# Kernel tuning notes

Hardware: AMD Instinct MI355X
Metric: run time of the kernel (lower is better)

Reference implementation:

```python
import jax, jax.numpy as jnp
import numpy as np

WS = (8, 8)
NUM_HEADS = 6
DIM = 192
HEAD_DIM = DIM // NUM_HEADS
SCALE = HEAD_DIM ** -0.5


def _relative_position_index(ws):
    ch, cw = np.arange(ws[0]), np.arange(ws[1])
    coords = np.stack(np.meshgrid(ch, cw, indexing='ij'))          # (2, Wh, Ww)
    cf = coords.reshape(2, -1)                                      # (2, N)
    rel = cf[:, :, None] - cf[:, None, :]                           # (2, N, N)
    rel = rel.transpose(1, 2, 0).copy()                             # (N, N, 2)
    rel[:, :, 0] += ws[0] - 1
    rel[:, :, 1] += ws[1] - 1
    rel[:, :, 0] *= 2 * ws[1] - 1
    return rel.sum(-1)                                              # (N, N)

REL_IDX = jnp.asarray(_relative_position_index(WS))


def setup_inputs() -> dict:
    key = jax.random.key(0)
    ks = jax.random.split(key, 9)
    B_, N, C = 8192, WS[0] * WS[1], DIM
    x1 = jax.random.normal(ks[0], (B_, N, C), jnp.float32)
    x2 = jax.random.normal(ks[1], (B_, N, C), jnp.float32)
    mask = jnp.zeros((1024, N, N), jnp.float32)
    q_w = jax.random.normal(ks[2], (C, C), jnp.float32) * 0.02
    q_b = jnp.zeros((C,), jnp.float32)
    kv_w = jax.random.normal(ks[3], (2 * C, C), jnp.float32) * 0.02
    kv_b = jnp.zeros((2 * C,), jnp.float32)
    proj_w = jax.random.normal(ks[4], (C, C), jnp.float32) * 0.02
    proj_b = jnp.zeros((C,), jnp.float32)
    table = jax.random.normal(ks[5], ((2 * WS[0] - 1) * (2 * WS[1] - 1), NUM_HEADS), jnp.float32) * 0.02
    return dict(x1=x1, x2=x2, mask=mask, q_w=q_w, q_b=q_b, kv_w=kv_w,
                kv_b=kv_b, proj_w=proj_w, proj_b=proj_b, table=table)


def reference(x1, x2, mask, q_w, q_b, kv_w, kv_b, proj_w, proj_b, table):
    B_, N, C = x1.shape
    H, hd = NUM_HEADS, HEAD_DIM
    q = (x1 @ q_w.T + q_b).reshape(B_, N, H, hd).transpose(0, 2, 1, 3)   # (B_,H,N,hd)
    kv = (x2 @ kv_w.T + kv_b).reshape(B_, N, 2, H, hd).transpose(2, 0, 3, 1, 4)
    k, v = kv[0], kv[1]                                                   # (B_,H,N,hd)
    attn = jnp.einsum('bhnd,bhmd->bhnm', q * SCALE, k)                    # (B_,H,N,N)
    bias = table[REL_IDX.reshape(-1)].reshape(N, N, H).transpose(2, 0, 1)  # (H,N,N)
    attn = attn + bias[None]
    nW = mask.shape[0]
    attn = attn.reshape(B_ // nW, nW, H, N, N) + mask[None, :, None]
    attn = jax.nn.softmax(attn.reshape(B_, H, N, N), axis=-1)
    out = jnp.einsum('bhnm,bhmd->bhnd', attn, v).transpose(0, 2, 1, 3).reshape(B_, N, C)
    return out @ proj_w.T + proj_b
```

## Files before the change

kernel.cpp:

```cpp
#include <hip/hip_runtime.h>

typedef __bf16 bf16_t;
typedef __bf16 bf16x8 __attribute__((ext_vector_type(8)));
typedef __bf16 bf16x4 __attribute__((ext_vector_type(4)));
typedef __bf16 bf16x2 __attribute__((ext_vector_type(2)));
typedef float f32x4 __attribute__((ext_vector_type(4)));

#define SCALE 0.17677669529663687f

__device__ __forceinline__ f32x4 mfma16(bf16x8 a, bf16x8 b, f32x4 c) {
  return __builtin_amdgcn_mfma_f32_16x16x32_bf16(a, b, c, 0, 0, 0);
}

__device__ __forceinline__ int swz(int row, int colByte, int strideB) {
  return row * strideB + ((((colByte >> 4) ^ (row & 7)) << 4) | (colByte & 15));
}

__device__ __forceinline__ void barrier_nd() {
  asm volatile("s_waitcnt lgkmcnt(0)" ::: "memory");
  __builtin_amdgcn_s_barrier();
  asm volatile("" ::: "memory");
}

union CvtU { bf16x2 h; unsigned int u; };
union PaU { unsigned int u[4]; bf16x8 v; };

__global__ void prep(const float* __restrict__ qw, const float* __restrict__ kvw,
                     const float* __restrict__ pw, bf16_t* __restrict__ wsb) {
  int i = blockIdx.x * 256 + threadIdx.x;
#pragma unroll
  for (int j = 0; j < 4; ++j) {
    int e = i * 4 + j;
    float v;
    if (e < 36864) v = qw[e] * SCALE;
    else if (e < 110592) v = kvw[e - 36864];
    else v = pw[e - 110592];
    wsb[e] = (bf16_t)v;
  }
}

template <bool WS>
__device__ __forceinline__ bf16x8 ldw(const bf16_t* __restrict__ wb,
                                      const float* __restrict__ wf, int off) {
  if constexpr (WS) {
    return *(const bf16x8*)(wb + off);
  } else {
    const float4* p = (const float4*)(wf + off);
    float4 a = p[0], c = p[1];
    bf16x8 r;
    r[0] = (bf16_t)a.x; r[1] = (bf16_t)a.y; r[2] = (bf16_t)a.z; r[3] = (bf16_t)a.w;
    r[4] = (bf16_t)c.x; r[5] = (bf16_t)c.y; r[6] = (bf16_t)c.z; r[7] = (bf16_t)c.w;
    return r;
  }
}

template <bool WS>
__global__ __launch_bounds__(512, 2) void wca_main(
    const float* __restrict__ x1, const float* __restrict__ x2,
    const float* __restrict__ mask,
    const float* __restrict__ qw_f, const float* __restrict__ qb,
    const float* __restrict__ kvw_f, const float* __restrict__ kvb,
    const float* __restrict__ pw_f, const float* __restrict__ pb,
    const float* __restrict__ table,
    const bf16_t* __restrict__ wsb,
    float* __restrict__ out) {
  extern __shared__ char smem[];
  char* RA = smem;
  char* RK = smem + 49152;
  char* RV = smem + 98304;

  const int t = threadIdx.x;
  const int w = t >> 6, l = t & 63, lo = l & 15, hi = l >> 4;
  const int win0 = 2 * blockIdx.x;

  const bf16_t* q_wb = wsb;
  const bf16_t* kv_wb = wsb + 36864;
  const bf16_t* p_wb = wsb + 110592;

  {
    const float4* s2a = (const float4*)(x2 + (size_t)win0 * 12288);
    const float4* s2b = (const float4*)(x2 + (size_t)(win0 + 1) * 12288);
    float4 ld[12];
#pragma unroll
    for (int it = 0; it < 3; ++it) {
      int idx = it * 512 + t;
      ld[4 * it + 0] = s2a[2 * idx]; ld[4 * it + 1] = s2a[2 * idx + 1];
      ld[4 * it + 2] = s2b[2 * idx]; ld[4 * it + 3] = s2b[2 * idx + 1];
    }
#pragma unroll
    for (int it = 0; it < 3; ++it) {
      int idx = it * 512 + t;
      int n = idx / 24, g = idx - n * 24;
      bf16x8 v;
      float4 a = ld[4 * it + 0], c = ld[4 * it + 1];
      v[0] = (bf16_t)a.x; v[1] = (bf16_t)a.y; v[2] = (bf16_t)a.z; v[3] = (bf16_t)a.w;
      v[4] = (bf16_t)c.x; v[5] = (bf16_t)c.y; v[6] = (bf16_t)c.z; v[7] = (bf16_t)c.w;
      *(bf16x8*)(RA + swz(n, g * 16, 384)) = v;
      a = ld[4 * it + 2]; c = ld[4 * it + 3];
      v[0] = (bf16_t)a.x; v[1] = (bf16_t)a.y; v[2] = (bf16_t)a.z; v[3] = (bf16_t)a.w;
      v[4] = (bf16_t)c.x; v[5] = (bf16_t)c.y; v[6] = (bf16_t)c.z; v[7] = (bf16_t)c.w;
      *(bf16x8*)(RA + swz(64 + n, g * 16, 384)) = v;
    }
  }
  barrier_nd();

  {
    bf16x8 wA[6][3];
#pragma unroll
    for (int kk = 0; kk < 6; ++kk)
#pragma unroll
      for (int ct = 0; ct < 3; ++ct) {
        int row = w * 48 + ct * 16 + lo;
        wA[kk][ct] = ldw<WS>(kv_wb, kvw_f, row * 192 + kk * 32 + hi * 8);
      }
    for (int wv = 0; wv < 2; ++wv) {
      f32x4 acc[4][3];
#pragma unroll
      for (int rt = 0; rt < 4; ++rt)
#pragma unroll
        for (int ct = 0; ct < 3; ++ct) { f32x4 z = {0.f, 0.f, 0.f, 0.f}; acc[rt][ct] = z; }
#pragma unroll
      for (int kk = 0; kk < 6; ++kk) {
        bf16x8 a[4];
#pragma unroll
        for (int rt = 0; rt < 4; ++rt)
          a[rt] = *(const bf16x8*)(RA + swz(wv * 64 + rt * 16 + lo, (kk * 4 + hi) * 16, 384));
#pragma unroll
        for (int rt = 0; rt < 4; ++rt)
#pragma unroll
          for (int ct = 0; ct < 3; ++ct)
            acc[rt][ct] = mfma16(a[rt], wA[kk][ct], acc[rt][ct]);
      }
      if (w < 4) {
#pragma unroll
        for (int ct = 0; ct < 3; ++ct) {
          int och = w * 48 + ct * 16 + lo;
          float bv = kvb[och];
#pragma unroll
          for (int rt = 0; rt < 4; ++rt)
#pragma unroll
            for (int i = 0; i < 4; ++i)
              *(bf16_t*)(RK + swz(wv * 64 + rt * 16 + hi * 4 + i, och * 2, 384)) =
                  (bf16_t)(acc[rt][ct][i] + bv);
        }
      } else {
#pragma unroll
        for (int ct = 0; ct < 3; ++ct) {
          int och = (w - 4) * 48 + ct * 16 + lo;
          float bv = kvb[192 + och];
#pragma unroll
          for (int rt = 0; rt < 4; ++rt) {
            int n0 = rt * 16 + hi * 4;
            bf16x4 pk;
#pragma unroll
            for (int i = 0; i < 4; ++i) pk[i] = (bf16_t)(acc[rt][ct][i] + bv);
            *(bf16x4*)(RV + wv * 24576 + swz(och, n0 * 2, 128)) = pk;
          }
        }
      }
    }
  }
  barrier_nd();

  {
    const int wv = w >> 2, rt2 = (w >> 1) & 1, cg = w & 1;
    const float* x1w = x1 + (size_t)(win0 + wv) * 12288;
    f32x4 acc[2][6];
#pragma unroll
    for (int rt = 0; rt < 2; ++rt)
#pragma unroll
      for (int ct = 0; ct < 6; ++ct) { f32x4 z = {0.f, 0.f, 0.f, 0.f}; acc[rt][ct] = z; }
#pragma unroll
    for (int kh = 0; kh < 2; ++kh) {
      float4 xf[2][3][2];
#pragma unroll
      for (int rt = 0; rt < 2; ++rt) {
        const float4* p = (const float4*)(x1w + (rt2 * 32 + rt * 16 + lo) * 192);
#pragma unroll
        for (int k2 = 0; k2 < 3; ++k2) {
          xf[rt][k2][0] = p[(kh * 3 + k2) * 8 + hi * 2];
          xf[rt][k2][1] = p[(kh * 3 + k2) * 8 + hi * 2 + 1];
        }
      }
      bf16x8 wB[3][6];
#pragma unroll
      for (int k2 = 0; k2 < 3; ++k2)
#pragma unroll
        for (int ct = 0; ct < 6; ++ct) {
          int col = cg * 96 + ct * 16 + lo;
          wB[k2][ct] = ldw<WS>(q_wb, qw_f, col * 192 + (kh * 3 + k2) * 32 + hi * 8);
        }
#pragma unroll
      for (int k2 = 0; k2 < 3; ++k2)
#pragma unroll
        for (int rt = 0; rt < 2; ++rt) {
          bf16x8 a;
          float4 xa = xf[rt][k2][0], xb = xf[rt][k2][1];
          a[0] = (bf16_t)xa.x; a[1] = (bf16_t)xa.y; a[2] = (bf16_t)xa.z; a[3] = (bf16_t)xa.w;
          a[4] = (bf16_t)xb.x; a[5] = (bf16_t)xb.y; a[6] = (bf16_t)xb.z; a[7] = (bf16_t)xb.w;
#pragma unroll
          for (int ct = 0; ct < 6; ++ct) acc[rt][ct] = mfma16(a, wB[k2][ct], acc[rt][ct]);
        }
    }
#pragma unroll
    for (int ct = 0; ct < 6; ++ct) {
      int col = cg * 96 + ct * 16 + lo;
      float qbs = qb[col] * SCALE;
#pragma unroll
      for (int rt = 0; rt < 2; ++rt)
#pragma unroll
        for (int i = 0; i < 4; ++i) {
          int row = wv * 64 + rt2 * 32 + rt * 16 + hi * 4 + i;
          float val = WS ? (acc[rt][ct][i] + qbs) : (acc[rt][ct][i] + qb[col]) * SCALE;
          *(bf16_t*)(RA + swz(row, col * 2, 384)) = (bf16_t)val;
        }
    }
  }
  barrier_nd();

  {
    const int wv = w >> 2, rt32 = (w >> 1) & 1, hh = w & 1;
    const int win = win0 + wv;
    const float* maskb = mask + (size_t)(win & 1023) * 4096;
    f32x4 mk[2][4];
    int ridx[2][4][4];
#pragma unroll
    for (int rts = 0; rts < 2; ++rts) {
      int r = rt32 * 32 + rts * 16 + lo;
#pragma unroll
      for (int ct = 0; ct < 4; ++ct) {
        mk[rts][ct] = *(const f32x4*)(maskb + r * 64 + ct * 16 + hi * 4);
#pragma unroll
        for (int i = 0; i < 4; ++i) {
          int c = ct * 16 + hi * 4 + i;
          ridx[rts][ct][i] = (((r >> 3) - (c >> 3) + 7) * 15 + ((r & 7) - (c & 7) + 7)) * 6;
        }
      }
    }
#pragma unroll
    for (int hq = 0; hq < 3; ++hq) {
      const int h = hh * 3 + hq;
#pragma unroll
      for (int rts = 0; rts < 2; ++rts) {
        const int rbase = rt32 * 32 + rts * 16;
        const int r = rbase + lo;
        bf16x8 qa = *(const bf16x8*)(RA + swz(wv * 64 + r, h * 64 + hi * 16, 384));
        f32x4 s[4];
#pragma unroll
        for (int ct = 0; ct < 4; ++ct) {
          f32x4 ci;
#pragma unroll
          for (int i = 0; i < 4; ++i) ci[i] = table[ridx[rts][ct][i] + h];
          ci += mk[rts][ct];
          bf16x8 ka = *(const bf16x8*)(RK + swz(wv * 64 + ct * 16 + lo, h * 64 + hi * 16, 384));
          s[ct] = mfma16(ka, qa, ci);
        }
        float mx = -1e30f;
#pragma unroll
        for (int ct = 0; ct < 4; ++ct)
#pragma unroll
          for (int i = 0; i < 4; ++i) mx = fmaxf(mx, s[ct][i]);
        mx = fmaxf(mx, __shfl_xor(mx, 16));
        mx = fmaxf(mx, __shfl_xor(mx, 32));
        float sum = 0.f;
#pragma unroll
        for (int ct = 0; ct < 4; ++ct)
#pragma unroll
          for (int i = 0; i < 4; ++i) {
            float p = __expf(s[ct][i] - mx);
            s[ct][i] = p;
            sum += p;
          }
        sum += __shfl_xor(sum, 16);
        sum += __shfl_xor(sum, 32);
        float rinv = 1.0f / sum;
        unsigned int word[4][2];
#pragma unroll
        for (int ct = 0; ct < 4; ++ct)
#pragma unroll
          for (int i2 = 0; i2 < 2; ++i2) {
            CvtU cu;
            cu.h[0] = (bf16_t)(s[ct][2 * i2] * rinv);
            cu.h[1] = (bf16_t)(s[ct][2 * i2 + 1] * rinv);
            word[ct][i2] = cu.u;
          }
        f32x4 o0 = {0.f, 0.f, 0.f, 0.f}, o1 = {0.f, 0.f, 0.f, 0.f};
#pragma unroll
        for (int k2 = 0; k2 < 2; ++k2) {
          PaU pa;
#pragma unroll
          for (int j2 = 0; j2 < 4; ++j2) {
            int src = lo + ((hi & 1) << 5) + ((j2 >> 1) << 4);
            unsigned int wa = (unsigned int)__shfl((int)word[2 * k2][j2 & 1], src);
            unsigned int wb = (unsigned int)__shfl((int)word[2 * k2 + 1][j2 & 1], src);
            pa.u[j2] = (hi & 2) ? wb : wa;
          }
          bf16x8 v0 = *(const bf16x8*)(RV + wv * 24576 + swz(h * 32 + lo, k2 * 64 + hi * 16, 128));
          bf16x8 v1 = *(const bf16x8*)(RV + wv * 24576 + swz(h * 32 + 16 + lo, k2 * 64 + hi * 16, 128));
          o0 = mfma16(pa.v, v0, o0);
          o1 = mfma16(pa.v, v1, o1);
        }
#pragma unroll
        for (int i = 0; i < 4; ++i) {
          int rr = wv * 64 + rbase + hi * 4 + i;
          *(bf16_t*)(RA + swz(rr, h * 64 + lo * 2, 384)) = (bf16_t)o0[i];
          *(bf16_t*)(RA + swz(rr, h * 64 + 32 + lo * 2, 384)) = (bf16_t)o1[i];
        }
      }
    }
  }
  barrier_nd();

  {
    const int wv = w >> 2, cgo = w & 3;
    bf16x8 wO[6][3];
#pragma unroll
    for (int kk = 0; kk < 6; ++kk)
#pragma unroll
      for (int ct = 0; ct < 3; ++ct) {
        int col = cgo * 48 + ct * 16 + lo;
        wO[kk][ct] = ldw<WS>(p_wb, pw_f, col * 192 + kk * 32 + hi * 8);
      }
    f32x4 acc[4][3];
#pragma unroll
    for (int rt = 0; rt < 4; ++rt)
#pragma unroll
      for (int ct = 0; ct < 3; ++ct) { f32x4 z = {0.f, 0.f, 0.f, 0.f}; acc[rt][ct] = z; }
#pragma unroll
    for (int kk = 0; kk < 6; ++kk) {
      bf16x8 a[4];
#pragma unroll
      for (int rt = 0; rt < 4; ++rt)
        a[rt] = *(const bf16x8*)(RA + swz(wv * 64 + rt * 16 + lo, (kk * 4 + hi) * 16, 384));
#pragma unroll
      for (int rt = 0; rt < 4; ++rt)
#pragma unroll
        for (int ct = 0; ct < 3; ++ct)
          acc[rt][ct] = mfma16(a[rt], wO[kk][ct], acc[rt][ct]);
    }
    float* outp = out + (size_t)(win0 + wv) * 12288;
#pragma unroll
    for (int ct = 0; ct < 3; ++ct) {
      int col = cgo * 48 + ct * 16 + lo;
      float bv = pb[col];
#pragma unroll
      for (int rt = 0; rt < 4; ++rt)
#pragma unroll
        for (int i = 0; i < 4; ++i)
          outp[(rt * 16 + hi * 4 + i) * 192 + col] = acc[rt][ct][i] + bv;
    }
  }
}

extern "C" void kernel_launch(void* const* d_in, const int* in_sizes, int n_in,
                              void* d_out, int out_size, void* d_ws, size_t ws_size,
                              hipStream_t stream) {
  const float* x1 = (const float*)d_in[0];
  const float* x2 = (const float*)d_in[1];
  const float* mask = (const float*)d_in[2];
  const float* qw = (const float*)d_in[3];
  const float* qb = (const float*)d_in[4];
  const float* kvw = (const float*)d_in[5];
  const float* kvb = (const float*)d_in[6];
  const float* pw = (const float*)d_in[7];
  const float* pb = (const float*)d_in[8];
  const float* table = (const float*)d_in[9];
  float* out = (float*)d_out;
  bf16_t* wsb = (bf16_t*)d_ws;
  const int LDS_BYTES = 147456;
  if (ws_size >= 294912) {
    prep<<<144, 256, 0, stream>>>(qw, kvw, pw, wsb);
    wca_main<true><<<4096, 512, LDS_BYTES, stream>>>(x1, x2, mask, qw, qb, kvw, kvb,
                                                     pw, pb, table, wsb, out);
  } else {
    wca_main<false><<<4096, 512, LDS_BYTES, stream>>>(x1, x2, mask, qw, qb, kvw, kvb,
                                                      pw, pb, table, wsb, out);
  }
}
```

Measured before the change: 651.9 us.

## Prefetch x1 during KV GEMM, transpose MFMA outputs for vector LDS stores, drop barrier

Half of the x1 tile for the Q projection is now loaded into registers during the KV projection phase, so its global latency overlaps with that phase's MFMAs. The mask loads are moved into the Q GEMM. Several MFMAs swap operand order so each lane holds four consecutive columns, which turns scalar bf16 LDS stores into packed bf16x4 stores for K, Q and attention output. The barrier between Q projection and attention is removed, since each wave now reads only the Q rows it wrote itself. This adds register pressure under launch_bounds(512,2), and the relative-position indices are recomputed inline instead of being precomputed.

```diff
diff --git a/kernel.cpp b/kernel.cpp
--- a/kernel.cpp
+++ b/kernel.cpp
@@ -72,6 +72,7 @@
   const int t = threadIdx.x;
   const int w = t >> 6, l = t & 63, lo = l & 15, hi = l >> 4;
   const int win0 = 2 * blockIdx.x;
+  const int wvB = w >> 2, rt2 = (w >> 1) & 1, hh = w & 1;
 
   const bf16_t* q_wb = wsb;
   const bf16_t* kv_wb = wsb + 36864;
@@ -104,15 +105,30 @@
   }
   barrier_nd();
 
+  float4 xp[12];
   {
+    const int part = w >> 2;
+    const int kcol = (w & 3) * 48;
     bf16x8 wA[6][3];
 #pragma unroll
     for (int kk = 0; kk < 6; ++kk)
 #pragma unroll
       for (int ct = 0; ct < 3; ++ct) {
-        int row = w * 48 + ct * 16 + lo;
+        int row = part * 192 + kcol + ct * 16 + lo;
         wA[kk][ct] = ldw<WS>(kv_wb, kvw_f, row * 192 + kk * 32 + hi * 8);
       }
+    {
+      const float* x1w = x1 + (size_t)(win0 + wvB) * 12288;
+#pragma unroll
+      for (int rt = 0; rt < 2; ++rt) {
+        const float4* p = (const float4*)(x1w + (rt2 * 32 + rt * 16 + lo) * 192);
+#pragma unroll
+        for (int k2 = 0; k2 < 3; ++k2) {
+          xp[rt * 6 + k2 * 2 + 0] = p[k2 * 8 + hi * 2];
+          xp[rt * 6 + k2 * 2 + 1] = p[k2 * 8 + hi * 2 + 1];
+        }
+      }
+    }
     for (int wv = 0; wv < 2; ++wv) {
       f32x4 acc[4][3];
 #pragma unroll
@@ -125,28 +141,37 @@
 #pragma unroll
         for (int rt = 0; rt < 4; ++rt)
           a[rt] = *(const bf16x8*)(RA + swz(wv * 64 + rt * 16 + lo, (kk * 4 + hi) * 16, 384));
-#pragma unroll
-        for (int rt = 0; rt < 4; ++rt)
-#pragma unroll
-          for (int ct = 0; ct < 3; ++ct)
-            acc[rt][ct] = mfma16(a[rt], wA[kk][ct], acc[rt][ct]);
-      }
-      if (w < 4) {
+        if (part == 0) {
+#pragma unroll
+          for (int rt = 0; rt < 4; ++rt)
+#pragma unroll
+            for (int ct = 0; ct < 3; ++ct)
+              acc[rt][ct] = mfma16(wA[kk][ct], a[rt], acc[rt][ct]);
+        } else {
+#pragma unroll
+          for (int rt = 0; rt < 4; ++rt)
+#pragma unroll
+            for (int ct = 0; ct < 3; ++ct)
+              acc[rt][ct] = mfma16(a[rt], wA[kk][ct], acc[rt][ct]);
+        }
+      }
+      if (part == 0) {
 #pragma unroll
         for (int ct = 0; ct < 3; ++ct) {
-          int och = w * 48 + ct * 16 + lo;
-          float bv = kvb[och];
-#pragma unroll
-          for (int rt = 0; rt < 4; ++rt)
-#pragma unroll
-            for (int i = 0; i < 4; ++i)
-              *(bf16_t*)(RK + swz(wv * 64 + rt * 16 + hi * 4 + i, och * 2, 384)) =
-                  (bf16_t)(acc[rt][ct][i] + bv);
+          f32x4 bv4 = *(const f32x4*)(kvb + kcol + ct * 16 + hi * 4);
+#pragma unroll
+          for (int rt = 0; rt < 4; ++rt) {
+            bf16x4 pk;
+#pragma unroll
+            for (int i = 0; i < 4; ++i) pk[i] = (bf16_t)(acc[rt][ct][i] + bv4[i]);
+            *(bf16x4*)(RK + swz(wv * 64 + rt * 16 + lo,
+                                kcol * 2 + ct * 32 + hi * 8, 384)) = pk;
+          }
         }
       } else {
 #pragma unroll
         for (int ct = 0; ct < 3; ++ct) {
-          int och = (w - 4) * 48 + ct * 16 + lo;
+          int och = kcol + ct * 16 + lo;
           float bv = kvb[192 + och];
 #pragma unroll
           for (int rt = 0; rt < 4; ++rt) {
@@ -162,97 +187,117 @@
   }
   barrier_nd();
 
+  f32x4 mk[2][4];
   {
-    const int wv = w >> 2, rt2 = (w >> 1) & 1, cg = w & 1;
-    const float* x1w = x1 + (size_t)(win0 + wv) * 12288;
+    const float* x1w = x1 + (size_t)(win0 + wvB) * 12288;
+    float4 xq[12];
+#pragma unroll
+    for (int rt = 0; rt < 2; ++rt) {
+      const float4* p = (const float4*)(x1w + (rt2 * 32 + rt * 16 + lo) * 192);
+#pragma unroll
+      for (int k2 = 0; k2 < 3; ++k2) {
+        xq[rt * 6 + k2 * 2 + 0] = p[(3 + k2) * 8 + hi * 2];
+        xq[rt * 6 + k2 * 2 + 1] = p[(3 + k2) * 8 + hi * 2 + 1];
+      }
+    }
     f32x4 acc[2][6];
 #pragma unroll
     for (int rt = 0; rt < 2; ++rt)
 #pragma unroll
       for (int ct = 0; ct < 6; ++ct) { f32x4 z = {0.f, 0.f, 0.f, 0.f}; acc[rt][ct] = z; }
-#pragma unroll
-    for (int kh = 0; kh < 2; ++kh) {
-      float4 xf[2][3][2];
-#pragma unroll
-      for (int rt = 0; rt < 2; ++rt) {
-        const float4* p = (const float4*)(x1w + (rt2 * 32 + rt * 16 + lo) * 192);
-#pragma unroll
-        for (int k2 = 0; k2 < 3; ++k2) {
-          xf[rt][k2][0] = p[(kh * 3 + k2) * 8 + hi * 2];
-          xf[rt][k2][1] = p[(kh * 3 + k2) * 8 + hi * 2 + 1];
-        }
-      }
+    {
       bf16x8 wB[3][6];
 #pragma unroll
       for (int k2 = 0; k2 < 3; ++k2)
 #pragma unroll
         for (int ct = 0; ct < 6; ++ct) {
-          int col = cg * 96 + ct * 16 + lo;
-          wB[k2][ct] = ldw<WS>(q_wb, qw_f, col * 192 + (kh * 3 + k2) * 32 + hi * 8);
+          int col = hh * 96 + ct * 16 + lo;
+          wB[k2][ct] = ldw<WS>(q_wb, qw_f, col * 192 + k2 * 32 + hi * 8);
         }
 #pragma unroll
       for (int k2 = 0; k2 < 3; ++k2)
 #pragma unroll
         for (int rt = 0; rt < 2; ++rt) {
+          float4 xa = xp[rt * 6 + k2 * 2], xb = xp[rt * 6 + k2 * 2 + 1];
           bf16x8 a;
-          float4 xa = xf[rt][k2][0], xb = xf[rt][k2][1];
           a[0] = (bf16_t)xa.x; a[1] = (bf16_t)xa.y; a[2] = (bf16_t)xa.z; a[3] = (bf16_t)xa.w;
           a[4] = (bf16_t)xb.x; a[5] = (bf16_t)xb.y; a[6] = (bf16_t)xb.z; a[7] = (bf16_t)xb.w;
 #pragma unroll
-          for (int ct = 0; ct < 6; ++ct) acc[rt][ct] = mfma16(a, wB[k2][ct], acc[rt][ct]);
+          for (int ct = 0; ct < 6; ++ct)
+            acc[rt][ct] = mfma16(wB[k2][ct], a, acc[rt][ct]);
+        }
+    }
+    {
+      const float* maskb = mask + (size_t)((win0 + wvB) & 1023) * 4096;
+#pragma unroll
+      for (int rts = 0; rts < 2; ++rts) {
+        int r = rt2 * 32 + rts * 16 + lo;
+#pragma unroll
+        for (int ct = 0; ct < 4; ++ct)
+          mk[rts][ct] = *(const f32x4*)(maskb + r * 64 + ct * 16 + hi * 4);
+      }
+    }
+    {
+      bf16x8 wB[3][6];
+#pragma unroll
+      for (int k2 = 0; k2 < 3; ++k2)
+#pragma unroll
+        for (int ct = 0; ct < 6; ++ct) {
+          int col = hh * 96 + ct * 16 + lo;
+          wB[k2][ct] = ldw<WS>(q_wb, qw_f, col * 192 + (3 + k2) * 32 + hi * 8);
+        }
+#pragma unroll
+      for (int k2 = 0; k2 < 3; ++k2)
+#pragma unroll
+        for (int rt = 0; rt < 2; ++rt) {
+          float4 xa = xq[rt * 6 + k2 * 2], xb = xq[rt * 6 + k2 * 2 + 1];
+          bf16x8 a;
+          a[0] = (bf16_t)xa.x; a[1] = (bf16_t)xa.y; a[2] = (bf16_t)xa.z; a[3] = (bf16_t)xa.w;
+          a[4] = (bf16_t)xb.x; a[5] = (bf16_t)xb.y; a[6] = (bf16_t)xb.z; a[7] = (bf16_t)xb.w;
+#pragma unroll
+          for (int ct = 0; ct < 6; ++ct)
+            acc[rt][ct] = mfma16(wB[k2][ct], a, acc[rt][ct]);
         }
     }
 #pragma unroll
     for (int ct = 0; ct < 6; ++ct) {
-      int col = cg * 96 + ct * 16 + lo;
-      float qbs = qb[col] * SCALE;
-#pragma unroll
-      for (int rt = 0; rt < 2; ++rt)
+      f32x4 qb4 = *(const f32x4*)(qb + hh * 96 + ct * 16 + hi * 4);
+#pragma unroll
+      for (int rt = 0; rt < 2; ++rt) {
+        int row = wvB * 64 + rt2 * 32 + rt * 16 + lo;
+        bf16x4 pk;
 #pragma unroll
         for (int i = 0; i < 4; ++i) {
-          int row = wv * 64 + rt2 * 32 + rt * 16 + hi * 4 + i;
-          float val = WS ? (acc[rt][ct][i] + qbs) : (acc[rt][ct][i] + qb[col]) * SCALE;
-          *(bf16_t*)(RA + swz(row, col * 2, 384)) = (bf16_t)val;
-        }
-    }
-  }
-  barrier_nd();
+          float val = WS ? (acc[rt][ct][i] + qb4[i] * SCALE)
+                         : (acc[rt][ct][i] + qb4[i]) * SCALE;
+          pk[i] = (bf16_t)val;
+        }
+        *(bf16x4*)(RA + swz(row, hh * 192 + ct * 32 + hi * 8, 384)) = pk;
+      }
+    }
+  }
 
   {
-    const int wv = w >> 2, rt32 = (w >> 1) & 1, hh = w & 1;
-    const int win = win0 + wv;
-    const float* maskb = mask + (size_t)(win & 1023) * 4096;
-    f32x4 mk[2][4];
-    int ridx[2][4][4];
-#pragma unroll
-    for (int rts = 0; rts < 2; ++rts) {
-      int r = rt32 * 32 + rts * 16 + lo;
-#pragma unroll
-      for (int ct = 0; ct < 4; ++ct) {
-        mk[rts][ct] = *(const f32x4*)(maskb + r * 64 + ct * 16 + hi * 4);
-#pragma unroll
-        for (int i = 0; i < 4; ++i) {
-          int c = ct * 16 + hi * 4 + i;
-          ridx[rts][ct][i] = (((r >> 3) - (c >> 3) + 7) * 15 + ((r & 7) - (c & 7) + 7)) * 6;
-        }
-      }
-    }
 #pragma unroll
     for (int hq = 0; hq < 3; ++hq) {
       const int h = hh * 3 + hq;
 #pragma unroll
       for (int rts = 0; rts < 2; ++rts) {
-        const int rbase = rt32 * 32 + rts * 16;
+        const int rbase = rt2 * 32 + rts * 16;
         const int r = rbase + lo;
-        bf16x8 qa = *(const bf16x8*)(RA + swz(wv * 64 + r, h * 64 + hi * 16, 384));
+        bf16x8 qa = *(const bf16x8*)(RA + swz(wvB * 64 + r, h * 64 + hi * 16, 384));
         f32x4 s[4];
 #pragma unroll
         for (int ct = 0; ct < 4; ++ct) {
           f32x4 ci;
 #pragma unroll
-          for (int i = 0; i < 4; ++i) ci[i] = table[ridx[rts][ct][i] + h];
+          for (int i = 0; i < 4; ++i) {
+            int c = ct * 16 + hi * 4 + i;
+            int rel = (((r >> 3) - (c >> 3) + 7) * 15 + ((r & 7) - (c & 7) + 7)) * 6;
+            ci[i] = table[rel + h];
+          }
           ci += mk[rts][ct];
-          bf16x8 ka = *(const bf16x8*)(RK + swz(wv * 64 + ct * 16 + lo, h * 64 + hi * 16, 384));
+          bf16x8 ka = *(const bf16x8*)(RK + swz(wvB * 64 + ct * 16 + lo, h * 64 + hi * 16, 384));
           s[ct] = mfma16(ka, qa, ci);
         }
         float mx = -1e30f;
@@ -295,17 +340,16 @@
             unsigned int wb = (unsigned int)__shfl((int)word[2 * k2 + 1][j2 & 1], src);
             pa.u[j2] = (hi & 2) ? wb : wa;
           }
-          bf16x8 v0 = *(const bf16x8*)(RV + wv * 24576 + swz(h * 32 + lo, k2 * 64 + hi * 16, 128));
-          bf16x8 v1 = *(const bf16x8*)(RV + wv * 24576 + swz(h * 32 + 16 + lo, k2 * 64 + hi * 16, 128));
-          o0 = mfma16(pa.v, v0, o0);
-          o1 = mfma16(pa.v, v1, o1);
-        }
-#pragma unroll
-        for (int i = 0; i < 4; ++i) {
-          int rr = wv * 64 + rbase + hi * 4 + i;
-          *(bf16_t*)(RA + swz(rr, h * 64 + lo * 2, 384)) = (bf16_t)o0[i];
-          *(bf16_t*)(RA + swz(rr, h * 64 + 32 + lo * 2, 384)) = (bf16_t)o1[i];
-        }
+          bf16x8 v0 = *(const bf16x8*)(RV + wvB * 24576 + swz(h * 32 + lo, k2 * 64 + hi * 16, 128));
+          bf16x8 v1 = *(const bf16x8*)(RV + wvB * 24576 + swz(h * 32 + 16 + lo, k2 * 64 + hi * 16, 128));
+          o0 = mfma16(v0, pa.v, o0);
+          o1 = mfma16(v1, pa.v, o1);
+        }
+        bf16x4 p0, p1;
+#pragma unroll
+        for (int i = 0; i < 4; ++i) { p0[i] = (bf16_t)o0[i]; p1[i] = (bf16_t)o1[i]; }
+        *(bf16x4*)(RA + swz(wvB * 64 + r, h * 64 + hi * 8, 384)) = p0;
+        *(bf16x4*)(RA + swz(wvB * 64 + r, h * 64 + 32 + hi * 8, 384)) = p1;
       }
     }
   }
```

Result: slower. 720.7 us (+10.5%).

## Make kernel persistent with producer warps double-buffering next window's inputs

Applied to the files above, without the earlier changes.

Replaces the one-block-per-two-windows launch with 256 persistent blocks that each loop over 32 windows. Two warps act as producers, converting the next window's x1/x2 to bf16 in double-buffered LDS while six compute warps run KV projection, Q projection, attention and output projection on the current window. This aims to overlap global-load latency with MFMA work and to amortize launch and setup costs. In exchange it drops to 256 blocks, which may leave CUs underused on a 256-CU part at two blocks per CU. Compute warps also reload weights every iteration, and only six of eight warps do math.

```diff
diff --git a/kernel.cpp b/kernel.cpp
--- a/kernel.cpp
+++ b/kernel.cpp
@@ -65,88 +65,92 @@
     const bf16_t* __restrict__ wsb,
     float* __restrict__ out) {
   extern __shared__ char smem[];
-  char* RA = smem;
-  char* RK = smem + 49152;
-  char* RV = smem + 98304;
+  char* RK = smem + 98304;
+  char* RV = smem + 122880;
 
   const int t = threadIdx.x;
   const int w = t >> 6, l = t & 63, lo = l & 15, hi = l >> 4;
-  const int win0 = 2 * blockIdx.x;
+  const int bid = blockIdx.x;
 
   const bf16_t* q_wb = wsb;
   const bf16_t* kv_wb = wsb + 36864;
   const bf16_t* p_wb = wsb + 110592;
 
-  {
-    const float4* s2a = (const float4*)(x2 + (size_t)win0 * 12288);
-    const float4* s2b = (const float4*)(x2 + (size_t)(win0 + 1) * 12288);
-    float4 ld[12];
-#pragma unroll
-    for (int it = 0; it < 3; ++it) {
-      int idx = it * 512 + t;
-      ld[4 * it + 0] = s2a[2 * idx]; ld[4 * it + 1] = s2a[2 * idx + 1];
-      ld[4 * it + 2] = s2b[2 * idx]; ld[4 * it + 3] = s2b[2 * idx + 1];
+  const int rb = (w >= 3 && w < 6) ? 1 : 0;
+  const int cg3 = w - rb * 3;
+
+  if (w >= 6) {
+    const int L = (w - 6) * 64 + l;
+    const float4* s2 = (const float4*)(x2 + (size_t)(bid * 32) * 12288);
+    const float4* s1 = (const float4*)(x1 + (size_t)(bid * 32) * 12288);
+#pragma unroll
+    for (int ch = 0; ch < 12; ++ch) {
+      int G = ch * 128 + L;
+      int n = G / 24, g = G - n * 24;
+      float4 a = s2[2 * G], b = s2[2 * G + 1];
+      bf16x8 v;
+      v[0] = (bf16_t)a.x; v[1] = (bf16_t)a.y; v[2] = (bf16_t)a.z; v[3] = (bf16_t)a.w;
+      v[4] = (bf16_t)b.x; v[5] = (bf16_t)b.y; v[6] = (bf16_t)b.z; v[7] = (bf16_t)b.w;
+      *(bf16x8*)(smem + swz(n, g * 16, 384)) = v;
+      a = s1[2 * G]; b = s1[2 * G + 1];
+      v[0] = (bf16_t)a.x; v[1] = (bf16_t)a.y; v[2] = (bf16_t)a.z; v[3] = (bf16_t)a.w;
+      v[4] = (bf16_t)b.x; v[5] = (bf16_t)b.y; v[6] = (bf16_t)b.z; v[7] = (bf16_t)b.w;
+      *(bf16x8*)(smem + 49152 + swz(n, g * 16, 384)) = v;
     }
-#pragma unroll
-    for (int it = 0; it < 3; ++it) {
-      int idx = it * 512 + t;
-      int n = idx / 24, g = idx - n * 24;
-      bf16x8 v;
-      float4 a = ld[4 * it + 0], c = ld[4 * it + 1];
-      v[0] = (bf16_t)a.x; v[1] = (bf16_t)a.y; v[2] = (bf16_t)a.z; v[3] = (bf16_t)a.w;
-      v[4] = (bf16_t)c.x; v[5] = (bf16_t)c.y; v[6] = (bf16_t)c.z; v[7] = (bf16_t)c.w;
-      *(bf16x8*)(RA + swz(n, g * 16, 384)) = v;
-      a = ld[4 * it + 2]; c = ld[4 * it + 3];
-      v[0] = (bf16_t)a.x; v[1] = (bf16_t)a.y; v[2] = (bf16_t)a.z; v[3] = (bf16_t)a.w;
-      v[4] = (bf16_t)c.x; v[5] = (bf16_t)c.y; v[6] = (bf16_t)c.z; v[7] = (bf16_t)c.w;
-      *(bf16x8*)(RA + swz(64 + n, g * 16, 384)) = v;
-    }
   }
   barrier_nd();
 
-  {
-    bf16x8 wA[6][3];
-#pragma unroll
-    for (int kk = 0; kk < 6; ++kk)
-#pragma unroll
-      for (int ct = 0; ct < 3; ++ct) {
-        int row = w * 48 + ct * 16 + lo;
-        wA[kk][ct] = ldw<WS>(kv_wb, kvw_f, row * 192 + kk * 32 + hi * 8);
-      }
-    for (int wv = 0; wv < 2; ++wv) {
-      f32x4 acc[4][3];
+#pragma unroll 1
+  for (int j = 0; j < 32; ++j) {
+    const int win = bid * 32 + j;
+    const int cur = j & 1;
+    char* xin = smem + cur * 24576;
+    const char* x1s = smem + 49152 + cur * 24576;
+
+    if (w < 6) {
+      const int part = (w >= 3) ? 1 : 0;
+      const int kcol = cg3 * 64;
+      bf16x8 wA[6][4];
+#pragma unroll
+      for (int kk = 0; kk < 6; ++kk)
+#pragma unroll
+        for (int ct = 0; ct < 4; ++ct) {
+          int row = part * 192 + kcol + ct * 16 + lo;
+          wA[kk][ct] = ldw<WS>(kv_wb, kvw_f, row * 192 + kk * 32 + hi * 8);
+        }
+      f32x4 acc[4][4];
 #pragma unroll
       for (int rt = 0; rt < 4; ++rt)
 #pragma unroll
-        for (int ct = 0; ct < 3; ++ct) { f32x4 z = {0.f, 0.f, 0.f, 0.f}; acc[rt][ct] = z; }
+        for (int ct = 0; ct < 4; ++ct) { f32x4 z = {0.f, 0.f, 0.f, 0.f}; acc[rt][ct] = z; }
 #pragma unroll
       for (int kk = 0; kk < 6; ++kk) {
         bf16x8 a[4];
 #pragma unroll
         for (int rt = 0; rt < 4; ++rt)
-          a[rt] = *(const bf16x8*)(RA + swz(wv * 64 + rt * 16 + lo, (kk * 4 + hi) * 16, 384));
+          a[rt] = *(const bf16x8*)(xin + swz(rt * 16 + lo, (kk * 4 + hi) * 16, 384));
 #pragma unroll
         for (int rt = 0; rt < 4; ++rt)
 #pragma unroll
-          for (int ct = 0; ct < 3; ++ct)
+          for (int ct = 0; ct < 4; ++ct)
             acc[rt][ct] = mfma16(a[rt], wA[kk][ct], acc[rt][ct]);
       }
-      if (w < 4) {
-#pragma unroll
-        for (int ct = 0; ct < 3; ++ct) {
-          int och = w * 48 + ct * 16 + lo;
+      if (part == 0) {
+#pragma unroll
+        for (int ct = 0; ct < 4; ++ct) {
+          int och = kcol + ct * 16 + lo;
           float bv = kvb[och];
 #pragma unroll
           for (int rt = 0; rt < 4; ++rt)
 #pragma unroll
             for (int i = 0; i < 4; ++i)
-              *(bf16_t*)(RK + swz(wv * 64 + rt * 16 + hi * 4 + i, och * 2, 384)) =
+              *(bf16_t*)(RK + swz(rt * 16 + hi * 4 + i, och * 2, 384)) =
                   (bf16_t)(acc[rt][ct][i] + bv);
         }
       } else {
 #pragma unroll
-        for (int ct = 0; ct < 3; ++ct) {
-          int och = (w - 4) * 48 + ct * 16 + lo;
+        for (int ct = 0; ct < 4; ++ct) {
+          int och = kcol + ct * 16 + lo;
           float bv = kvb[192 + och];
 #pragma unroll
           for (int rt = 0; rt < 4; ++rt) {
@@ -154,200 +158,204 @@
             bf16x4 pk;
 #pragma unroll
             for (int i = 0; i < 4; ++i) pk[i] = (bf16_t)(acc[rt][ct][i] + bv);
-            *(bf16x4*)(RV + wv * 24576 + swz(och, n0 * 2, 128)) = pk;
+            *(bf16x4*)(RV + swz(och, n0 * 2, 128)) = pk;
           }
         }
       }
     }
-  }
-  barrier_nd();
-
-  {
-    const int wv = w >> 2, rt2 = (w >> 1) & 1, cg = w & 1;
-    const float* x1w = x1 + (size_t)(win0 + wv) * 12288;
-    f32x4 acc[2][6];
-#pragma unroll
-    for (int rt = 0; rt < 2; ++rt)
-#pragma unroll
-      for (int ct = 0; ct < 6; ++ct) { f32x4 z = {0.f, 0.f, 0.f, 0.f}; acc[rt][ct] = z; }
-#pragma unroll
-    for (int kh = 0; kh < 2; ++kh) {
-      float4 xf[2][3][2];
-#pragma unroll
-      for (int rt = 0; rt < 2; ++rt) {
-        const float4* p = (const float4*)(x1w + (rt2 * 32 + rt * 16 + lo) * 192);
-#pragma unroll
-        for (int k2 = 0; k2 < 3; ++k2) {
-          xf[rt][k2][0] = p[(kh * 3 + k2) * 8 + hi * 2];
-          xf[rt][k2][1] = p[(kh * 3 + k2) * 8 + hi * 2 + 1];
-        }
-      }
-      bf16x8 wB[3][6];
-#pragma unroll
-      for (int k2 = 0; k2 < 3; ++k2)
-#pragma unroll
-        for (int ct = 0; ct < 6; ++ct) {
-          int col = cg * 96 + ct * 16 + lo;
-          wB[k2][ct] = ldw<WS>(q_wb, qw_f, col * 192 + (kh * 3 + k2) * 32 + hi * 8);
-        }
-#pragma unroll
-      for (int k2 = 0; k2 < 3; ++k2)
-#pragma unroll
-        for (int rt = 0; rt < 2; ++rt) {
-          bf16x8 a;
-          float4 xa = xf[rt][k2][0], xb = xf[rt][k2][1];
-          a[0] = (bf16_t)xa.x; a[1] = (bf16_t)xa.y; a[2] = (bf16_t)xa.z; a[3] = (bf16_t)xa.w;
-          a[4] = (bf16_t)xb.x; a[5] = (bf16_t)xb.y; a[6] = (bf16_t)xb.z; a[7] = (bf16_t)xb.w;
-#pragma unroll
-          for (int ct = 0; ct < 6; ++ct) acc[rt][ct] = mfma16(a, wB[k2][ct], acc[rt][ct]);
-        }
+    barrier_nd();
+
+    if (w < 6) {
+      {
+        bf16x8 wB[6][4];
+#pragma unroll
+        for (int kk = 0; kk < 6; ++kk)
+#pragma unroll
+          for (int ct = 0; ct < 4; ++ct) {
+            int col = cg3 * 64 + ct * 16 + lo;
+            wB[kk][ct] = ldw<WS>(q_wb, qw_f, col * 192 + kk * 32 + hi * 8);
+          }
+        f32x4 acc[2][4];
+#pragma unroll
+        for (int rt = 0; rt < 2; ++rt)
+#pragma unroll
+          for (int ct = 0; ct < 4; ++ct) { f32x4 z = {0.f, 0.f, 0.f, 0.f}; acc[rt][ct] = z; }
+#pragma unroll
+        for (int kk = 0; kk < 6; ++kk) {
+          bf16x8 a[2];
+#pragma unroll
+          for (int rt = 0; rt < 2; ++rt)
+            a[rt] = *(const bf16x8*)(x1s + swz(rb * 32 + rt * 16 + lo, (kk * 4 + hi) * 16, 384));
+#pragma unroll
+          for (int rt = 0; rt < 2; ++rt)
+#pragma unroll
+            for (int ct = 0; ct < 4; ++ct)
+              acc[rt][ct] = mfma16(a[rt], wB[kk][ct], acc[rt][ct]);
+        }
+#pragma unroll
+        for (int ct = 0; ct < 4; ++ct) {
+          int col = cg3 * 64 + ct * 16 + lo;
+          float qv = qb[col];
+#pragma unroll
+          for (int rt = 0; rt < 2; ++rt)
+#pragma unroll
+            for (int i = 0; i < 4; ++i) {
+              int row = rb * 32 + rt * 16 + hi * 4 + i;
+              float val = WS ? (acc[rt][ct][i] + qv * SCALE)
+                             : (acc[rt][ct][i] + qv) * SCALE;
+              *(bf16_t*)(xin + swz(row, col * 2, 384)) = (bf16_t)val;
+            }
+        }
+      }
+      {
+        const float* maskb = mask + (size_t)(win & 1023) * 4096;
+        f32x4 mk[2][4];
+        int ridx[2][4][4];
+#pragma unroll
+        for (int rts = 0; rts < 2; ++rts) {
+          int r = rb * 32 + rts * 16 + lo;
+#pragma unroll
+          for (int ct = 0; ct < 4; ++ct) {
+            mk[rts][ct] = *(const f32x4*)(maskb + r * 64 + ct * 16 + hi * 4);
+#pragma unroll
+            for (int i = 0; i < 4; ++i) {
+              int cc = ct * 16 + hi * 4 + i;
+              ridx[rts][ct][i] = (((r >> 3) - (cc >> 3) + 7) * 15 + ((r & 7) - (cc & 7) + 7)) * 6;
+            }
+          }
+        }
+#pragma unroll
+        for (int hq = 0; hq < 2; ++hq) {
+          const int h = cg3 * 2 + hq;
+#pragma unroll
+          for (int rts = 0; rts < 2; ++rts) {
+            const int rbase = rb * 32 + rts * 16;
+            const int r = rbase + lo;
+            bf16x8 qa = *(const bf16x8*)(xin + swz(r, h * 64 + hi * 16, 384));
+            f32x4 s[4];
+#pragma unroll
+            for (int ct = 0; ct < 4; ++ct) {
+              f32x4 ci;
+#pragma unroll
+              for (int i = 0; i < 4; ++i) ci[i] = table[ridx[rts][ct][i] + h];
+              ci += mk[rts][ct];
+              bf16x8 ka = *(const bf16x8*)(RK + swz(ct * 16 + lo, h * 64 + hi * 16, 384));
+              s[ct] = mfma16(ka, qa, ci);
+            }
+            float mx = -1e30f;
+#pragma unroll
+            for (int ct = 0; ct < 4; ++ct)
+#pragma unroll
+              for (int i = 0; i < 4; ++i) mx = fmaxf(mx, s[ct][i]);
+            mx = fmaxf(mx, __shfl_xor(mx, 16));
+            mx = fmaxf(mx, __shfl_xor(mx, 32));
+            float sum = 0.f;
+#pragma unroll
+            for (int ct = 0; ct < 4; ++ct)
+#pragma unroll
+              for (int i = 0; i < 4; ++i) {
+                float p = __expf(s[ct][i] - mx);
+                s[ct][i] = p;
+                sum += p;
+              }
+            sum += __shfl_xor(sum, 16);
+            sum += __shfl_xor(sum, 32);
+            float rinv = 1.0f / sum;
+            unsigned int word[4][2];
+#pragma unroll
+            for (int ct = 0; ct < 4; ++ct)
+#pragma unroll
+              for (int i2 = 0; i2 < 2; ++i2) {
+                CvtU cu;
+                cu.h[0] = (bf16_t)(s[ct][2 * i2] * rinv);
+                cu.h[1] = (bf16_t)(s[ct][2 * i2 + 1] * rinv);
+                word[ct][i2] = cu.u;
+              }
+            f32x4 o0 = {0.f, 0.f, 0.f, 0.f}, o1 = {0.f, 0.f, 0.f, 0.f};
+#pragma unroll
+            for (int k2 = 0; k2 < 2; ++k2) {
+              PaU pa;
+#pragma unroll
+              for (int j2 = 0; j2 < 4; ++j2) {
+                int src = lo + ((hi & 1) << 5) + ((j2 >> 1) << 4);
+                unsigned int wa = (unsigned int)__shfl((int)word[2 * k2][j2 & 1], src);
+                unsigned int wb = (unsigned int)__shfl((int)word[2 * k2 + 1][j2 & 1], src);
+                pa.u[j2] = (hi & 2) ? wb : wa;
+              }
+              bf16x8 v0 = *(const bf16x8*)(RV + swz(h * 32 + lo, k2 * 64 + hi * 16, 128));
+              bf16x8 v1 = *(const bf16x8*)(RV + swz(h * 32 + 16 + lo, k2 * 64 + hi * 16, 128));
+              o0 = mfma16(pa.v, v0, o0);
+              o1 = mfma16(pa.v, v1, o1);
+            }
+#pragma unroll
+            for (int i = 0; i < 4; ++i) {
+              int rr = rbase + hi * 4 + i;
+              *(bf16_t*)(xin + swz(rr, h * 64 + lo * 2, 384)) = (bf16_t)o0[i];
+              *(bf16_t*)(xin + swz(rr, h * 64 + 32 + lo * 2, 384)) = (bf16_t)o1[i];
+            }
+          }
+        }
+      }
+    } else if (j < 31) {
+      const int L = (w - 6) * 64 + l;
+      char* xd = smem + (cur ^ 1) * 24576;
+      char* x1d = smem + 49152 + (cur ^ 1) * 24576;
+      const float4* s2 = (const float4*)(x2 + (size_t)(win + 1) * 12288);
+      const float4* s1 = (const float4*)(x1 + (size_t)(win + 1) * 12288);
+#pragma unroll
+      for (int ch = 0; ch < 12; ++ch) {
+        int G = ch * 128 + L;
+        int n = G / 24, g = G - n * 24;
+        float4 a = s2[2 * G], b = s2[2 * G + 1];
+        bf16x8 v;
+        v[0] = (bf16_t)a.x; v[1] = (bf16_t)a.y; v[2] = (bf16_t)a.z; v[3] = (bf16_t)a.w;
+        v[4] = (bf16_t)b.x; v[5] = (bf16_t)b.y; v[6] = (bf16_t)b.z; v[7] = (bf16_t)b.w;
+        *(bf16x8*)(xd + swz(n, g * 16, 384)) = v;
+        a = s1[2 * G]; b = s1[2 * G + 1];
+        v[0] = (bf16_t)a.x; v[1] = (bf16_t)a.y; v[2] = (bf16_t)a.z; v[3] = (bf16_t)a.w;
+        v[4] = (bf16_t)b.x; v[5] = (bf16_t)b.y; v[6] = (bf16_t)b.z; v[7] = (bf16_t)b.w;
+        *(bf16x8*)(x1d + swz(n, g * 16, 384)) = v;
+      }
     }
-#pragma unroll
-    for (int ct = 0; ct < 6; ++ct) {
-      int col = cg * 96 + ct * 16 + lo;
-      float qbs = qb[col] * SCALE;
+    barrier_nd();
+
+    if (w < 6) {
+      bf16x8 wO[6][4];
+#pragma unroll
+      for (int kk = 0; kk < 6; ++kk)
+#pragma unroll
+        for (int ct = 0; ct < 4; ++ct) {
+          int col = cg3 * 64 + ct * 16 + lo;
+          wO[kk][ct] = ldw<WS>(p_wb, pw_f, col * 192 + kk * 32 + hi * 8);
+        }
+      f32x4 acc[2][4];
 #pragma unroll
       for (int rt = 0; rt < 2; ++rt)
 #pragma unroll
-        for (int i = 0; i < 4; ++i) {
-          int row = wv * 64 + rt2 * 32 + rt * 16 + hi * 4 + i;
-          float val = WS ? (acc[rt][ct][i] + qbs) : (acc[rt][ct][i] + qb[col]) * SCALE;
-          *(bf16_t*)(RA + swz(row, col * 2, 384)) = (bf16_t)val;
-        }
-    }
-  }
-  barrier_nd();
-
-  {
-    const int wv = w >> 2, rt32 = (w >> 1) & 1, hh = w & 1;
-    const int win = win0 + wv;
-    const float* maskb = mask + (size_t)(win & 1023) * 4096;
-    f32x4 mk[2][4];
-    int ridx[2][4][4];
-#pragma unroll
-    for (int rts = 0; rts < 2; ++rts) {
-      int r = rt32 * 32 + rts * 16 + lo;
+        for (int ct = 0; ct < 4; ++ct) { f32x4 z = {0.f, 0.f, 0.f, 0.f}; acc[rt][ct] = z; }
+#pragma unroll
+      for (int kk = 0; kk < 6; ++kk) {
+        bf16x8 a[2];
+#pragma unroll
+        for (int rt = 0; rt < 2; ++rt)
+          a[rt] = *(const bf16x8*)(xin + swz(rb * 32 + rt * 16 + lo, (kk * 4 + hi) * 16, 384));
+#pragma unroll
+        for (int rt = 0; rt < 2; ++rt)
+#pragma unroll
+          for (int ct = 0; ct < 4; ++ct)
+            acc[rt][ct] = mfma16(a[rt], wO[kk][ct], acc[rt][ct]);
+      }
+      float* outp = out + (size_t)win * 12288;
 #pragma unroll
       for (int ct = 0; ct < 4; ++ct) {
-        mk[rts][ct] = *(const f32x4*)(maskb + r * 64 + ct * 16 + hi * 4);
-#pragma unroll
-        for (int i = 0; i < 4; ++i) {
-          int c = ct * 16 + hi * 4 + i;
-          ridx[rts][ct][i] = (((r >> 3) - (c >> 3) + 7) * 15 + ((r & 7) - (c & 7) + 7)) * 6;
-        }
-      }
-    }
-#pragma unroll
-    for (int hq = 0; hq < 3; ++hq) {
-      const int h = hh * 3 + hq;
-#pragma unroll
-      for (int rts = 0; rts < 2; ++rts) {
-        const int rbase = rt32 * 32 + rts * 16;
-        const int r = rbase + lo;
-        bf16x8 qa = *(const bf16x8*)(RA + swz(wv * 64 + r, h * 64 + hi * 16, 384));
-        f32x4 s[4];
-#pragma unroll
-        for (int ct = 0; ct < 4; ++ct) {
-          f32x4 ci;
-#pragma unroll
-          for (int i = 0; i < 4; ++i) ci[i] = table[ridx[rts][ct][i] + h];
-          ci += mk[rts][ct];
-          bf16x8 ka = *(const bf16x8*)(RK + swz(wv * 64 + ct * 16 + lo, h * 64 + hi * 16, 384));
-          s[ct] = mfma16(ka, qa, ci);
-        }
-        float mx = -1e30f;
-#pragma unroll
-        for (int ct = 0; ct < 4; ++ct)
-#pragma unroll
-          for (int i = 0; i < 4; ++i) mx = fmaxf(mx, s[ct][i]);
-        mx = fmaxf(mx, __shfl_xor(mx, 16));
-        mx = fmaxf(mx, __shfl_xor(mx, 32));
-        float sum = 0.f;
-#pragma unroll
-        for (int ct = 0; ct < 4; ++ct)
-#pragma unroll
-          for (int i = 0; i < 4; ++i) {
-            float p = __expf(s[ct][i] - mx);
-            s[ct][i] = p;
-            sum += p;
-          }
-        sum += __shfl_xor(sum, 16);
-        sum += __shfl_xor(sum, 32);
-        float rinv = 1.0f / sum;
-        unsigned int word[4][2];
-#pragma unroll
-        for (int ct = 0; ct < 4; ++ct)
-#pragma unroll
-          for (int i2 = 0; i2 < 2; ++i2) {
-            CvtU cu;
-            cu.h[0] = (bf16_t)(s[ct][2 * i2] * rinv);
-            cu.h[1] = (bf16_t)(s[ct][2 * i2 + 1] * rinv);
-            word[ct][i2] = cu.u;
-          }
-        f32x4 o0 = {0.f, 0.f, 0.f, 0.f}, o1 = {0.f, 0.f, 0.f, 0.f};
-#pragma unroll
-        for (int k2 = 0; k2 < 2; ++k2) {
-          PaU pa;
-#pragma unroll
-          for (int j2 = 0; j2 < 4; ++j2) {
-            int src = lo + ((hi & 1) << 5) + ((j2 >> 1) << 4);
-            unsigned int wa = (unsigned int)__shfl((int)word[2 * k2][j2 & 1], src);
-            unsigned int wb = (unsigned int)__shfl((int)word[2 * k2 + 1][j2 & 1], src);
-            pa.u[j2] = (hi & 2) ? wb : wa;
-          }
-          bf16x8 v0 = *(const bf16x8*)(RV + wv * 24576 + swz(h * 32 + lo, k2 * 64 + hi * 16, 128));
-          bf16x8 v1 = *(const bf16x8*)(RV + wv * 24576 + swz(h * 32 + 16 + lo, k2 * 64 + hi * 16, 128));
-          o0 = mfma16(pa.v, v0, o0);
-          o1 = mfma16(pa.v, v1, o1);
-        }
-#pragma unroll
-        for (int i = 0; i < 4; ++i) {
-          int rr = wv * 64 + rbase + hi * 4 + i;
-          *(bf16_t*)(RA + swz(rr, h * 64 + lo * 2, 384)) = (bf16_t)o0[i];
-          *(bf16_t*)(RA + swz(rr, h * 64 + 32 + lo * 2, 384)) = (bf16_t)o1[i];
-        }
-      }
-    }
-  }
-  barrier_nd();
-
-  {
-    const int wv = w >> 2, cgo = w & 3;
-    bf16x8 wO[6][3];
-#pragma unroll
-    for (int kk = 0; kk < 6; ++kk)
-#pragma unroll
-      for (int ct = 0; ct < 3; ++ct) {
-        int col = cgo * 48 + ct * 16 + lo;
-        wO[kk][ct] = ldw<WS>(p_wb, pw_f, col * 192 + kk * 32 + hi * 8);
-      }
-    f32x4 acc[4][3];
-#pragma unroll
-    for (int rt = 0; rt < 4; ++rt)
-#pragma unroll
-      for (int ct = 0; ct < 3; ++ct) { f32x4 z = {0.f, 0.f, 0.f, 0.f}; acc[rt][ct] = z; }
-#pragma unroll
-    for (int kk = 0; kk < 6; ++kk) {
-      bf16x8 a[4];
-#pragma unroll
-      for (int rt = 0; rt < 4; ++rt)
-        a[rt] = *(const bf16x8*)(RA + swz(wv * 64 + rt * 16 + lo, (kk * 4 + hi) * 16, 384));
-#pragma unroll
-      for (int rt = 0; rt < 4; ++rt)
-#pragma unroll
-        for (int ct = 0; ct < 3; ++ct)
-          acc[rt][ct] = mfma16(a[rt], wO[kk][ct], acc[rt][ct]);
-    }
-    float* outp = out + (size_t)(win0 + wv) * 12288;
-#pragma unroll
-    for (int ct = 0; ct < 3; ++ct) {
-      int col = cgo * 48 + ct * 16 + lo;
-      float bv = pb[col];
-#pragma unroll
-      for (int rt = 0; rt < 4; ++rt)
-#pragma unroll
-        for (int i = 0; i < 4; ++i)
-          outp[(rt * 16 + hi * 4 + i) * 192 + col] = acc[rt][ct][i] + bv;
+        int col = cg3 * 64 + ct * 16 + lo;
+        float bv = pb[col];
+#pragma unroll
+        for (int rt = 0; rt < 2; ++rt)
+#pragma unroll
+          for (int i = 0; i < 4; ++i)
+            outp[(rb * 32 + rt * 16 + hi * 4 + i) * 192 + col] = acc[rt][ct][i] + bv;
+      }
     }
   }
 }
@@ -370,10 +378,10 @@
   const int LDS_BYTES = 147456;
   if (ws_size >= 294912) {
     prep<<<144, 256, 0, stream>>>(qw, kvw, pw, wsb);
-    wca_main<true><<<4096, 512, LDS_BYTES, stream>>>(x1, x2, mask, qw, qb, kvw, kvb,
+    wca_main<true><<<256, 512, LDS_BYTES, stream>>>(x1, x2, mask, qw, qb, kvw, kvb,
+                                                    pw, pb, table, wsb, out);
+  } else {
+    wca_main<false><<<256, 512, LDS_BYTES, stream>>>(x1, x2, mask, qw, qb, kvw, kvb,
                                                      pw, pb, table, wsb, out);
-  } else {
-    wca_main<false><<<4096, 512, LDS_BYTES, stream>>>(x1, x2, mask, qw, qb, kvw, kvb,
-                                                      pw, pb, table, wsb, out);
-  }
-}
+  }
+}
```

Measured after the change: 1.422 ms. 2.18x slower.
